# Performance work log

Measured on AMD Instinct MI355X. Metric: run time of the kernel, lower is better.

## Reference

```python
import jax, jax.numpy as jnp
import numpy as np

BN_EPS = 1e-5
NUM_GRAPHS = 64

def _bn(h, gamma, beta):
    # BatchNorm1d over node dim, training-mode (batch statistics, biased var)
    mu = jnp.mean(h, axis=0)
    var = jnp.mean(jnp.square(h - mu), axis=0)
    return gamma * (h - mu) * jax.lax.rsqrt(var + BN_EPS) + beta

def _gin_conv(x, src, dst, Wa, ba, gamma, beta, Wb, bb):
    # sum-aggregate neighbor features: agg[v] = sum_{(u,v) in E} x[u]
    n = x.shape[0]
    agg = jax.ops.segment_sum(x[src], dst, num_segments=n)
    h = x + agg  # eps = 0 (default GINConv)
    h = jax.nn.relu(_bn(h @ Wa + ba, gamma, beta))
    return jax.nn.relu(h @ Wb + bb)

def setup_inputs() -> dict:
    key = jax.random.key(0)
    ks = jax.random.split(key, 16)
    N, E, IN, D, OUT = 50000, 800000, 128, 512, 10
    x = jax.random.normal(ks[0], (N, IN), dtype=jnp.float32)
    edge_index = jax.random.randint(ks[1], (2, E), 0, N, dtype=jnp.int64)
    batch = jnp.sort(jax.random.randint(ks[2], (N,), 0, NUM_GRAPHS, dtype=jnp.int64))
    def lin(k, i, o):
        return jax.random.normal(k, (i, o), dtype=jnp.float32) / np.sqrt(i)
    return {
        "x": x, "edge_index": edge_index, "batch": batch,
        "W1a": lin(ks[3], IN, D), "b1a": jnp.zeros((D,), jnp.float32),
        "g1": jnp.ones((D,), jnp.float32), "be1": jnp.zeros((D,), jnp.float32),
        "W1b": lin(ks[4], D, D), "b1b": jnp.zeros((D,), jnp.float32),
        "W2a": lin(ks[5], D, D), "b2a": jnp.zeros((D,), jnp.float32),
        "g2": jnp.ones((D,), jnp.float32), "be2": jnp.zeros((D,), jnp.float32),
        "W2b": lin(ks[6], D, D), "b2b": jnp.zeros((D,), jnp.float32),
        "Wl1": lin(ks[7], D, D), "bl1": jnp.zeros((D,), jnp.float32),
        "Wl2": lin(ks[8], D, OUT), "bl2": jnp.zeros((OUT,), jnp.float32),
    }

def reference(x, edge_index, batch, W1a, b1a, g1, be1, W1b, b1b,
              W2a, b2a, g2, be2, W2b, b2b, Wl1, bl1, Wl2, bl2):
    src, dst = edge_index[0], edge_index[1]
    h = _gin_conv(x, src, dst, W1a, b1a, g1, be1, W1b, b1b)
    h = _gin_conv(h, src, dst, W2a, b2a, g2, be2, W2b, b2b)
    pooled = jax.ops.segment_sum(h, batch, num_segments=NUM_GRAPHS)  # [G, D]
    out = jax.nn.relu(pooled @ Wl1 + bl1)
    return out @ Wl2 + bl2  # [G, out_channels]
```

## Files before the change

### kernel.cpp

```cpp
#include <hip/hip_runtime.h>
#include <cstdint>
#include <cstddef>

#define N_NODES  50000
#define N_EDGES  800000
#define DIM_IN   128
#define DIM_H    512
#define N_GRAPHS 64
#define DIM_OUT  10
#define BN_EPS   1e-5f
#define SCAN_B   196

typedef _Float16 h16;
using f16x8 = __attribute__((ext_vector_type(8))) _Float16;
using f32x4 = __attribute__((ext_vector_type(4))) float;

__device__ inline float4 add4(float4 a, float4 b) {
    return make_float4(a.x + b.x, a.y + b.y, a.z + b.z, a.w + b.w);
}

__global__ __launch_bounds__(256) void k_wcast_all(
    const float* __restrict__ W1a, const float* __restrict__ W1b,
    const float* __restrict__ W2a, const float* __restrict__ W2b,
    h16* __restrict__ Wt1a, h16* __restrict__ Wt1b,
    h16* __restrict__ Wt2a, h16* __restrict__ Wt2b)
{
    int b = blockIdx.x;
    const float* W; h16* Wt; int K, base;
    if (b < 32)       { W = W1a; Wt = Wt1a; K = DIM_IN; base = 0; }
    else if (b < 160) { W = W1b; Wt = Wt1b; K = DIM_H;  base = 32; }
    else if (b < 288) { W = W2a; Wt = Wt2a; K = DIM_H;  base = 160; }
    else              { W = W2b; Wt = Wt2b; K = DIM_H;  base = 288; }
    int t = (b - base) * 256 + threadIdx.x;
    int total = (K >> 3) * DIM_H;
    if (t >= total) return;
    int k8 = t / DIM_H;
    int n  = t - k8 * DIM_H;
    f16x8 o;
#pragma unroll
    for (int j = 0; j < 8; ++j)
        o[j] = (h16)W[(size_t)(k8 * 8 + j) * DIM_H + n];
    *reinterpret_cast<f16x8*>(&Wt[(size_t)n * K + k8 * 8]) = o;
}

__global__ __launch_bounds__(256) void k_deg(
    const int* __restrict__ dst, int* __restrict__ deg)
{
    int t = blockIdx.x * 256 + threadIdx.x;
    if (t < N_EDGES) atomicAdd(&deg[dst[t]], 1);
}

__global__ __launch_bounds__(256) void k_scan1(
    const int* __restrict__ deg, int* __restrict__ bsum)
{
    __shared__ int s[256];
    int tid = threadIdx.x;
    int i = blockIdx.x * 256 + tid;
    s[tid] = (i < N_NODES) ? deg[i] : 0;
    __syncthreads();
    for (int off = 128; off > 0; off >>= 1) {
        if (tid < off) s[tid] += s[tid + off];
        __syncthreads();
    }
    if (tid == 0) bsum[blockIdx.x] = s[0];
}

__global__ __launch_bounds__(256) void k_scan2(
    const int* __restrict__ bsum, int* __restrict__ boff)
{
    __shared__ int s[256];
    int tid = threadIdx.x;
    s[tid] = (tid < SCAN_B) ? bsum[tid] : 0;
    __syncthreads();
    for (int off = 1; off < 256; off <<= 1) {
        int u = (tid >= off) ? s[tid - off] : 0;
        __syncthreads();
        s[tid] += u;
        __syncthreads();
    }
    if (tid < SCAN_B) boff[tid] = (tid == 0) ? 0 : s[tid - 1];
}

__global__ __launch_bounds__(256) void k_scan3(
    const int* __restrict__ deg, const int* __restrict__ boff,
    int* __restrict__ rowptr, int* __restrict__ cursor)
{
    __shared__ int s[256];
    int tid = threadIdx.x;
    int i = blockIdx.x * 256 + tid;
    int v = (i < N_NODES) ? deg[i] : 0;
    s[tid] = v;
    __syncthreads();
    for (int off = 1; off < 256; off <<= 1) {
        int u = (tid >= off) ? s[tid - off] : 0;
        __syncthreads();
        s[tid] += u;
        __syncthreads();
    }
    int excl = s[tid] - v + boff[blockIdx.x];
    if (i < N_NODES) {
        rowptr[i] = excl;
        cursor[i] = excl;
        if (i == N_NODES - 1) rowptr[N_NODES] = excl + v;
    }
}

__global__ __launch_bounds__(256) void k_fill(
    const int* __restrict__ src, const int* __restrict__ dst,
    int* __restrict__ cursor, int* __restrict__ eidx)
{
    int t = blockIdx.x * 256 + threadIdx.x;
    if (t >= N_EDGES) return;
    int pos = atomicAdd(&cursor[dst[t]], 1);
    eidx[pos] = src[t];
}

__global__ __launch_bounds__(256) void k_gather128(
    const float4* __restrict__ X, const int* __restrict__ rowptr,
    const int* __restrict__ eidx, f16x8* __restrict__ out)
{
    int t = blockIdx.x * 256 + threadIdx.x;
    int v = t >> 4, lane = t & 15;
    if (v >= N_NODES) return;
    int r0 = rowptr[v], r1 = rowptr[v + 1];
    float4 a0 = X[(size_t)v * 32 + lane * 2];
    float4 a1 = X[(size_t)v * 32 + lane * 2 + 1];
    for (int j = r0; j < r1; ++j) {
        int s = eidx[j];
        a0 = add4(a0, X[(size_t)s * 32 + lane * 2]);
        a1 = add4(a1, X[(size_t)s * 32 + lane * 2 + 1]);
    }
    f16x8 o;
    o[0] = (h16)a0.x; o[1] = (h16)a0.y; o[2] = (h16)a0.z; o[3] = (h16)a0.w;
    o[4] = (h16)a1.x; o[5] = (h16)a1.y; o[6] = (h16)a1.z; o[7] = (h16)a1.w;
    out[(size_t)v * 16 + lane] = o;
}

__global__ __launch_bounds__(256) void k_gather512h(
    const f16x8* __restrict__ X, const int* __restrict__ rowptr,
    const int* __restrict__ eidx, f16x8* __restrict__ out)
{
    int t = blockIdx.x * 256 + threadIdx.x;
    int v = t >> 6, lane = t & 63;
    if (v >= N_NODES) return;
    int r0 = rowptr[v], r1 = rowptr[v + 1];
    f16x8 sv = X[(size_t)v * 64 + lane];
    float a[8];
#pragma unroll
    for (int i = 0; i < 8; ++i) a[i] = (float)sv[i];
    int j = r0;
    for (; j + 7 < r1; j += 8) {
        f16x8 b0 = X[(size_t)eidx[j]     * 64 + lane];
        f16x8 b1 = X[(size_t)eidx[j + 1] * 64 + lane];
        f16x8 b2 = X[(size_t)eidx[j + 2] * 64 + lane];
        f16x8 b3 = X[(size_t)eidx[j + 3] * 64 + lane];
        f16x8 b4 = X[(size_t)eidx[j + 4] * 64 + lane];
        f16x8 b5 = X[(size_t)eidx[j + 5] * 64 + lane];
        f16x8 b6 = X[(size_t)eidx[j + 6] * 64 + lane];
        f16x8 b7 = X[(size_t)eidx[j + 7] * 64 + lane];
#pragma unroll
        for (int i = 0; i < 8; ++i)
            a[i] += (((float)b0[i] + (float)b1[i]) + ((float)b2[i] + (float)b3[i]))
                  + (((float)b4[i] + (float)b5[i]) + ((float)b6[i] + (float)b7[i]));
    }
    for (; j + 1 < r1; j += 2) {
        f16x8 b0 = X[(size_t)eidx[j]     * 64 + lane];
        f16x8 b1 = X[(size_t)eidx[j + 1] * 64 + lane];
#pragma unroll
        for (int i = 0; i < 8; ++i) a[i] += (float)b0[i] + (float)b1[i];
    }
    if (j < r1) {
        f16x8 b = X[(size_t)eidx[j] * 64 + lane];
#pragma unroll
        for (int i = 0; i < 8; ++i) a[i] += (float)b[i];
    }
    f16x8 o;
#pragma unroll
    for (int i = 0; i < 8; ++i) o[i] = (h16)a[i];
    out[(size_t)v * 64 + lane] = o;
}

template<bool AFFINE, bool RELU, bool STATS>
__global__ __launch_bounds__(512) void k_gemm_mfma(
    const h16* __restrict__ A, const h16* __restrict__ Bt,
    const float* __restrict__ bias, const float* __restrict__ sA,
    const float* __restrict__ cA, h16* __restrict__ C,
    float* __restrict__ csum, float* __restrict__ csq,
    int M, int N, int K, int lda)
{
    __shared__ f16x8 As[2][128 * 4];
    __shared__ f16x8 Bs[2][256 * 4];

    const int tid  = threadIdx.x;
    const int lane = tid & 63;
    const int w    = tid >> 6;
    const int wr   = w >> 2;
    const int wc   = w & 3;
    const int l15  = lane & 15;
    const int lk   = lane >> 4;
    const int m0   = blockIdx.x * 128;
    const int n0   = blockIdx.y * 256;

    const int a_row = tid >> 2;
    const int kb    = tid & 3;
    const int aswz  = kb ^ (a_row & 3);
    int ar = m0 + a_row; if (ar >= M) ar = M - 1;
    const h16* aptr = A + (size_t)ar * lda + kb * 8;
    const int b_col = tid >> 2;
    const int bswz  = kb ^ (b_col & 3);
    const h16* bptr = Bt + (size_t)(n0 + b_col) * K + kb * 8;
    const size_t bstride = (size_t)128 * K;

    f32x4 acc[4][4];
#pragma unroll
    for (int m = 0; m < 4; ++m)
#pragma unroll
        for (int n = 0; n < 4; ++n)
            acc[m][n] = (f32x4){0.f, 0.f, 0.f, 0.f};

    f16x8 av, bw0, bw1;

    auto load_tile = [&](int k0) {
        av  = *reinterpret_cast<const f16x8*>(aptr + k0);
        if (AFFINE) {
            int kk = k0 + kb * 8;
            float4 s0 = *reinterpret_cast<const float4*>(&sA[kk]);
            float4 s1 = *reinterpret_cast<const float4*>(&sA[kk + 4]);
            float4 c0 = *reinterpret_cast<const float4*>(&cA[kk]);
            float4 c1 = *reinterpret_cast<const float4*>(&cA[kk + 4]);
            float sarr[8] = {s0.x, s0.y, s0.z, s0.w, s1.x, s1.y, s1.z, s1.w};
            float carr[8] = {c0.x, c0.y, c0.z, c0.w, c1.x, c1.y, c1.z, c1.w};
#pragma unroll
            for (int i = 0; i < 8; ++i)
                av[i] = (h16)fmaxf(fmaf((float)av[i], sarr[i], carr[i]), 0.f);
        }
        bw0 = *reinterpret_cast<const f16x8*>(bptr + k0);
        bw1 = *reinterpret_cast<const f16x8*>(bptr + bstride + k0);
    };

    load_tile(0);
    int cur = 0;

    for (int k0 = 0; k0 < K; k0 += 32) {
        As[cur][a_row * 4 + aswz]         = av;
        Bs[cur][b_col * 4 + bswz]         = bw0;
        Bs[cur][(b_col + 128) * 4 + bswz] = bw1;
        if (k0 + 32 < K) load_tile(k0 + 32);
        __syncthreads();

        f16x8 af[4], bf[4];
#pragma unroll
        for (int m = 0; m < 4; ++m) {
            int row = wr * 64 + m * 16 + l15;
            af[m] = As[cur][row * 4 + (lk ^ (row & 3))];
        }
#pragma unroll
        for (int n = 0; n < 4; ++n) {
            int col = wc * 64 + n * 16 + l15;
            bf[n] = Bs[cur][col * 4 + (lk ^ (col & 3))];
        }
#pragma unroll
        for (int m = 0; m < 4; ++m)
#pragma unroll
            for (int n = 0; n < 4; ++n)
                acc[m][n] = __builtin_amdgcn_mfma_f32_16x16x32_f16(
                    af[m], bf[n], acc[m][n], 0, 0, 0);
        cur ^= 1;
    }

#pragma unroll
    for (int n = 0; n < 4; ++n) {
        int col = n0 + wc * 64 + n * 16 + l15;
        float bb = bias[col];
        float sp = 0.f, qp = 0.f;
#pragma unroll
        for (int m = 0; m < 4; ++m) {
            int row0 = m0 + wr * 64 + m * 16 + lk * 4;
#pragma unroll
            for (int r = 0; r < 4; ++r) {
                int row = row0 + r;
                if (row < M) {
                    float v = acc[m][n][r] + bb;
                    if (STATS) { sp += v; qp += v * v; }
                    if (RELU) v = fmaxf(v, 0.f);
                    C[(size_t)row * N + col] = (h16)v;
                }
            }
        }
        if (STATS) {
            sp += __shfl_xor(sp, 16); qp += __shfl_xor(qp, 16);
            sp += __shfl_xor(sp, 32); qp += __shfl_xor(qp, 32);
            if (lk == 0) {
                atomicAdd(&csum[col], sp);
                atomicAdd(&csq[col], qp);
            }
        }
    }
}

__global__ void k_fold(const float* __restrict__ csum, const float* __restrict__ csq,
                       const float* __restrict__ g, const float* __restrict__ be,
                       float* __restrict__ sf, float* __restrict__ cf)
{
    int c = threadIdx.x;
    const float invM = 1.0f / (float)N_NODES;
    float mu  = csum[c] * invM;
    float var = csq[c] * invM - mu * mu;
    float s   = g[c] * rsqrtf(var + BN_EPS);
    sf[c] = s;
    cf[c] = be[c] - mu * s;
}

__global__ __launch_bounds__(256) void k_pool(
    const h16* __restrict__ H, const int* __restrict__ batch,
    float* __restrict__ pooled)
{
    __shared__ int bg[128];
    int base = blockIdx.x * 128;
    if (threadIdx.x < 128) {
        int r = base + threadIdx.x;
        bg[threadIdx.x] = (r < N_NODES) ? batch[r] : -1;
    }
    __syncthreads();
    int c0 = threadIdx.x;
    float a0 = 0.f, a1 = 0.f;
    int cur = bg[0];
    for (int r = 0; r < 128; ++r) {
        int g = bg[r];
        if (g < 0) break;
        if (g != cur) {
            atomicAdd(&pooled[cur * DIM_H + c0],       a0);
            atomicAdd(&pooled[cur * DIM_H + c0 + 256], a1);
            a0 = a1 = 0.f;
            cur = g;
        }
        size_t row = (size_t)(base + r);
        a0 += (float)H[row * DIM_H + c0];
        a1 += (float)H[row * DIM_H + c0 + 256];
    }
    if (cur >= 0) {
        atomicAdd(&pooled[cur * DIM_H + c0],       a0);
        atomicAdd(&pooled[cur * DIM_H + c0 + 256], a1);
    }
}

__global__ __launch_bounds__(512) void k_head1(
    const float* __restrict__ pooled, const float* __restrict__ W,
    const float* __restrict__ b, float* __restrict__ q)
{
    __shared__ float row[DIM_H];
    int g = blockIdx.x, c = threadIdx.x;
    row[c] = pooled[(size_t)g * DIM_H + c];
    __syncthreads();
    float acc = 0.f;
    for (int k = 0; k < DIM_H; ++k)
        acc = fmaf(row[k], W[(size_t)k * DIM_H + c], acc);
    q[(size_t)g * DIM_H + c] = fmaxf(acc + b[c], 0.f);
}

__global__ __launch_bounds__(256) void k_head2(
    const float* __restrict__ q, const float* __restrict__ W,
    const float* __restrict__ b, float* __restrict__ out)
{
    int t = blockIdx.x * 256 + threadIdx.x;
    if (t >= N_GRAPHS * DIM_OUT) return;
    int g = t / DIM_OUT, c = t % DIM_OUT;
    float acc = 0.f;
    for (int k = 0; k < DIM_H; ++k)
        acc = fmaf(q[(size_t)g * DIM_H + k], W[(size_t)k * DIM_OUT + c], acc);
    out[t] = acc + b[c];
}

extern "C" void kernel_launch(void* const* d_in, const int* in_sizes, int n_in,
                              void* d_out, int out_size, void* d_ws, size_t ws_size,
                              hipStream_t stream)
{
    const float* x   = (const float*)d_in[0];
    const int*   ei  = (const int*)d_in[1];
    const int*   src = ei;
    const int*   dst = ei + N_EDGES;
    const int*   batch = (const int*)d_in[2];
    const float* W1a = (const float*)d_in[3];
    const float* b1a = (const float*)d_in[4];
    const float* g1  = (const float*)d_in[5];
    const float* be1 = (const float*)d_in[6];
    const float* W1b = (const float*)d_in[7];
    const float* b1b = (const float*)d_in[8];
    const float* W2a = (const float*)d_in[9];
    const float* b2a = (const float*)d_in[10];
    const float* g2  = (const float*)d_in[11];
    const float* be2 = (const float*)d_in[12];
    const float* W2b = (const float*)d_in[13];
    const float* b2b = (const float*)d_in[14];
    const float* Wl1 = (const float*)d_in[15];
    const float* bl1 = (const float*)d_in[16];
    const float* Wl2 = (const float*)d_in[17];
    const float* bl2 = (const float*)d_in[18];

    char* ws = (char*)d_ws;
    const size_t ROW_H = (size_t)N_NODES * DIM_H * 2;

    if (ws_size < 110000000ull) {
        hipMemsetAsync(d_out, 0, (size_t)out_size * 4, stream);
        return;
    }
    h16* B1h = (h16*)(ws + 0);
    h16* B2h = (h16*)(ws + ROW_H);
    h16* XAh = B2h;
    char* cp  = ws + 2 * ROW_H;
    int* deg    = (int*)(cp + 0);
    int* rowptr = (int*)(cp + 200192);
    int* cursor = (int*)(cp + 400384);
    int* eidx   = (int*)(cp + 600576);
    char* sm    = cp + 3800576;
    float* csum   = (float*)(sm + 0);
    float* csq    = (float*)(sm + 2048);
    float* sf     = (float*)(sm + 4096);
    float* cf     = (float*)(sm + 6144);
    float* pooled = (float*)(sm + 8192);
    float* qbuf   = (float*)(sm + 8192 + 131072);
    char* wt = sm + 8192 + 2 * 131072;
    h16* Wt1a = (h16*)(wt);
    h16* Wt1b = (h16*)(wt + 131072);
    h16* Wt2a = (h16*)(wt + 131072 + 524288);
    h16* Wt2b = (h16*)(wt + 131072 + 2 * 524288);
    int* bsum = (int*)(wt + 131072 + 3 * 524288);
    int* boff = bsum + 256;

    const dim3 gemm_grid(391, 2);
    const int EB = (N_EDGES + 255) / 256;

    k_wcast_all<<<416, 256, 0, stream>>>(W1a, W1b, W2a, W2b,
                                         Wt1a, Wt1b, Wt2a, Wt2b);

    hipMemsetAsync(deg, 0, (size_t)N_NODES * 4, stream);
    k_deg<<<EB, 256, 0, stream>>>(dst, deg);
    k_scan1<<<SCAN_B, 256, 0, stream>>>(deg, bsum);
    k_scan2<<<1, 256, 0, stream>>>(bsum, boff);
    k_scan3<<<SCAN_B, 256, 0, stream>>>(deg, boff, rowptr, cursor);
    k_fill<<<EB, 256, 0, stream>>>(src, dst, cursor, eidx);

    k_gather128<<<(N_NODES * 16 + 255) / 256, 256, 0, stream>>>(
        (const float4*)x, rowptr, eidx, (f16x8*)XAh);
    hipMemsetAsync(csum, 0, 4096, stream);
    k_gemm_mfma<false, false, true><<<gemm_grid, 512, 0, stream>>>(
        XAh, Wt1a, b1a, nullptr, nullptr, B1h, csum, csq,
        N_NODES, DIM_H, DIM_IN, DIM_IN);
    k_fold<<<1, 512, 0, stream>>>(csum, csq, g1, be1, sf, cf);
    k_gemm_mfma<true, true, false><<<gemm_grid, 512, 0, stream>>>(
        B1h, Wt1b, b1b, sf, cf, B2h, nullptr, nullptr,
        N_NODES, DIM_H, DIM_H, DIM_H);

    k_gather512h<<<(N_NODES * 64) / 256, 256, 0, stream>>>(
        (const f16x8*)B2h, rowptr, eidx, (f16x8*)B1h);
    hipMemsetAsync(csum, 0, 4096, stream);
    k_gemm_mfma<false, false, true><<<gemm_grid, 512, 0, stream>>>(
        B1h, Wt2a, b2a, nullptr, nullptr, B2h, csum, csq,
        N_NODES, DIM_H, DIM_H, DIM_H);
    k_fold<<<1, 512, 0, stream>>>(csum, csq, g2, be2, sf, cf);
    k_gemm_mfma<true, true, false><<<gemm_grid, 512, 0, stream>>>(
        B2h, Wt2b, b2b, sf, cf, B1h, nullptr, nullptr,
        N_NODES, DIM_H, DIM_H, DIM_H);

    hipMemsetAsync(pooled, 0, (size_t)N_GRAPHS * DIM_H * 4, stream);
    k_pool<<<(N_NODES + 127) / 128, 256, 0, stream>>>(B1h, batch, pooled);
    k_head1<<<N_GRAPHS, 512, 0, stream>>>(pooled, Wl1, bl1, qbuf);
    k_head2<<<3, 256, 0, stream>>>(qbuf, Wl2, bl2, (float*)d_out);
}
```

Before: 643.5 us.

## Use direct global-to-LDS loads in GEMM and split BN affine into separate kernel

Measured after the change: 653.3 us. No clear change (+1.5%).

```diff
diff --git a/kernel.cpp b/kernel.cpp
--- a/kernel.cpp
+++ b/kernel.cpp
@@ -17,6 +17,12 @@
 
 __device__ inline float4 add4(float4 a, float4 b) {
     return make_float4(a.x + b.x, a.y + b.y, a.z + b.z, a.w + b.w);
+}
+
+__device__ inline void gll16(const void* g, void* l) {
+    __builtin_amdgcn_global_load_lds(
+        (const __attribute__((address_space(1))) void*)g,
+        (__attribute__((address_space(3))) void*)l, 16, 0, 0);
 }
 
 __global__ __launch_bounds__(256) void k_wcast_all(
@@ -180,16 +186,34 @@
     out[(size_t)v * 64 + lane] = o;
 }
 
-template<bool AFFINE, bool RELU, bool STATS>
+__global__ __launch_bounds__(256) void k_affine(
+    h16* __restrict__ T, const float* __restrict__ sf, const float* __restrict__ cf)
+{
+    int t = blockIdx.x * 256 + threadIdx.x;
+    if (t >= N_NODES * (DIM_H / 8)) return;
+    int col0 = (t & 63) * 8;
+    f16x8 v = *reinterpret_cast<const f16x8*>(&T[(size_t)t * 8]);
+    float4 s0 = *reinterpret_cast<const float4*>(&sf[col0]);
+    float4 s1 = *reinterpret_cast<const float4*>(&sf[col0 + 4]);
+    float4 c0 = *reinterpret_cast<const float4*>(&cf[col0]);
+    float4 c1 = *reinterpret_cast<const float4*>(&cf[col0 + 4]);
+    float sarr[8] = {s0.x, s0.y, s0.z, s0.w, s1.x, s1.y, s1.z, s1.w};
+    float carr[8] = {c0.x, c0.y, c0.z, c0.w, c1.x, c1.y, c1.z, c1.w};
+#pragma unroll
+    for (int i = 0; i < 8; ++i)
+        v[i] = (h16)fmaxf(fmaf((float)v[i], sarr[i], carr[i]), 0.f);
+    *reinterpret_cast<f16x8*>(&T[(size_t)t * 8]) = v;
+}
+
+template<bool RELU, bool STATS>
 __global__ __launch_bounds__(512) void k_gemm_mfma(
     const h16* __restrict__ A, const h16* __restrict__ Bt,
-    const float* __restrict__ bias, const float* __restrict__ sA,
-    const float* __restrict__ cA, h16* __restrict__ C,
+    const float* __restrict__ bias, h16* __restrict__ C,
     float* __restrict__ csum, float* __restrict__ csq,
     int M, int N, int K, int lda)
 {
-    __shared__ f16x8 As[2][128 * 4];
-    __shared__ f16x8 Bs[2][256 * 4];
+    __shared__ f16x8 As[128 * 4];
+    __shared__ f16x8 Bs[256 * 4];
 
     const int tid  = threadIdx.x;
     const int lane = tid & 63;
@@ -201,15 +225,22 @@
     const int m0   = blockIdx.x * 128;
     const int n0   = blockIdx.y * 256;
 
-    const int a_row = tid >> 2;
-    const int kb    = tid & 3;
-    const int aswz  = kb ^ (a_row & 3);
+    int sA_ = w * 64 + lane;
+    int a_row = sA_ >> 2;
+    int a_kb  = (sA_ & 3) ^ (a_row & 3);
     int ar = m0 + a_row; if (ar >= M) ar = M - 1;
-    const h16* aptr = A + (size_t)ar * lda + kb * 8;
-    const int b_col = tid >> 2;
-    const int bswz  = kb ^ (b_col & 3);
-    const h16* bptr = Bt + (size_t)(n0 + b_col) * K + kb * 8;
-    const size_t bstride = (size_t)128 * K;
+    const h16* aSrc = A + (size_t)ar * lda + a_kb * 8;
+    f16x8* aBase = &As[w * 64];
+    int sB1 = w * 64 + lane;
+    int b1_col = sB1 >> 2;
+    int b1_kb  = (sB1 & 3) ^ (b1_col & 3);
+    const h16* bSrc1 = Bt + (size_t)(n0 + b1_col) * K + b1_kb * 8;
+    f16x8* bBase1 = &Bs[w * 64];
+    int sB2 = 512 + w * 64 + lane;
+    int b2_col = sB2 >> 2;
+    int b2_kb  = (sB2 & 3) ^ (b2_col & 3);
+    const h16* bSrc2 = Bt + (size_t)(n0 + b2_col) * K + b2_kb * 8;
+    f16x8* bBase2 = &Bs[512 + w * 64];
 
     f32x4 acc[4][4];
 #pragma unroll
@@ -218,46 +249,23 @@
         for (int n = 0; n < 4; ++n)
             acc[m][n] = (f32x4){0.f, 0.f, 0.f, 0.f};
 
-    f16x8 av, bw0, bw1;
-
-    auto load_tile = [&](int k0) {
-        av  = *reinterpret_cast<const f16x8*>(aptr + k0);
-        if (AFFINE) {
-            int kk = k0 + kb * 8;
-            float4 s0 = *reinterpret_cast<const float4*>(&sA[kk]);
-            float4 s1 = *reinterpret_cast<const float4*>(&sA[kk + 4]);
-            float4 c0 = *reinterpret_cast<const float4*>(&cA[kk]);
-            float4 c1 = *reinterpret_cast<const float4*>(&cA[kk + 4]);
-            float sarr[8] = {s0.x, s0.y, s0.z, s0.w, s1.x, s1.y, s1.z, s1.w};
-            float carr[8] = {c0.x, c0.y, c0.z, c0.w, c1.x, c1.y, c1.z, c1.w};
-#pragma unroll
-            for (int i = 0; i < 8; ++i)
-                av[i] = (h16)fmaxf(fmaf((float)av[i], sarr[i], carr[i]), 0.f);
-        }
-        bw0 = *reinterpret_cast<const f16x8*>(bptr + k0);
-        bw1 = *reinterpret_cast<const f16x8*>(bptr + bstride + k0);
-    };
-
-    load_tile(0);
-    int cur = 0;
-
     for (int k0 = 0; k0 < K; k0 += 32) {
-        As[cur][a_row * 4 + aswz]         = av;
-        Bs[cur][b_col * 4 + bswz]         = bw0;
-        Bs[cur][(b_col + 128) * 4 + bswz] = bw1;
-        if (k0 + 32 < K) load_tile(k0 + 32);
+        __syncthreads();
+        gll16(aSrc + k0, aBase);
+        gll16(bSrc1 + k0, bBase1);
+        gll16(bSrc2 + k0, bBase2);
         __syncthreads();
 
         f16x8 af[4], bf[4];
 #pragma unroll
         for (int m = 0; m < 4; ++m) {
             int row = wr * 64 + m * 16 + l15;
-            af[m] = As[cur][row * 4 + (lk ^ (row & 3))];
+            af[m] = As[row * 4 + (lk ^ (row & 3))];
         }
 #pragma unroll
         for (int n = 0; n < 4; ++n) {
             int col = wc * 64 + n * 16 + l15;
-            bf[n] = Bs[cur][col * 4 + (lk ^ (col & 3))];
+            bf[n] = Bs[col * 4 + (lk ^ (col & 3))];
         }
 #pragma unroll
         for (int m = 0; m < 4; ++m)
@@ -265,7 +273,6 @@
             for (int n = 0; n < 4; ++n)
                 acc[m][n] = __builtin_amdgcn_mfma_f32_16x16x32_f16(
                     af[m], bf[n], acc[m][n], 0, 0, 0);
-        cur ^= 1;
     }
 
 #pragma unroll
@@ -429,6 +436,7 @@
 
     const dim3 gemm_grid(391, 2);
     const int EB = (N_EDGES + 255) / 256;
+    const int AFB = (N_NODES * (DIM_H / 8) + 255) / 256;
 
     k_wcast_all<<<416, 256, 0, stream>>>(W1a, W1b, W2a, W2b,
                                          Wt1a, Wt1b, Wt2a, Wt2b);
@@ -443,24 +451,22 @@
     k_gather128<<<(N_NODES * 16 + 255) / 256, 256, 0, stream>>>(
         (const float4*)x, rowptr, eidx, (f16x8*)XAh);
     hipMemsetAsync(csum, 0, 4096, stream);
-    k_gemm_mfma<false, false, true><<<gemm_grid, 512, 0, stream>>>(
-        XAh, Wt1a, b1a, nullptr, nullptr, B1h, csum, csq,
-        N_NODES, DIM_H, DIM_IN, DIM_IN);
+    k_gemm_mfma<false, true><<<gemm_grid, 512, 0, stream>>>(
+        XAh, Wt1a, b1a, B1h, csum, csq, N_NODES, DIM_H, DIM_IN, DIM_IN);
     k_fold<<<1, 512, 0, stream>>>(csum, csq, g1, be1, sf, cf);
-    k_gemm_mfma<true, true, false><<<gemm_grid, 512, 0, stream>>>(
-        B1h, Wt1b, b1b, sf, cf, B2h, nullptr, nullptr,
-        N_NODES, DIM_H, DIM_H, DIM_H);
+    k_affine<<<AFB, 256, 0, stream>>>(B1h, sf, cf);
+    k_gemm_mfma<true, false><<<gemm_grid, 512, 0, stream>>>(
+        B1h, Wt1b, b1b, B2h, nullptr, nullptr, N_NODES, DIM_H, DIM_H, DIM_H);
 
     k_gather512h<<<(N_NODES * 64) / 256, 256, 0, stream>>>(
         (const f16x8*)B2h, rowptr, eidx, (f16x8*)B1h);
     hipMemsetAsync(csum, 0, 4096, stream);
-    k_gemm_mfma<false, false, true><<<gemm_grid, 512, 0, stream>>>(
-        B1h, Wt2a, b2a, nullptr, nullptr, B2h, csum, csq,
-        N_NODES, DIM_H, DIM_H, DIM_H);
+    k_gemm_mfma<false, true><<<gemm_grid, 512, 0, stream>>>(
+        B1h, Wt2a, b2a, B2h, csum, csq, N_NODES, DIM_H, DIM_H, DIM_H);
     k_fold<<<1, 512, 0, stream>>>(csum, csq, g2, be2, sf, cf);
-    k_gemm_mfma<true, true, false><<<gemm_grid, 512, 0, stream>>>(
-        B2h, Wt2b, b2b, sf, cf, B1h, nullptr, nullptr,
-        N_NODES, DIM_H, DIM_H, DIM_H);
+    k_affine<<<AFB, 256, 0, stream>>>(B2h, sf, cf);
+    k_gemm_mfma<true, false><<<gemm_grid, 512, 0, stream>>>(
+        B2h, Wt2b, b2b, B1h, nullptr, nullptr, N_NODES, DIM_H, DIM_H, DIM_H);
 
     hipMemsetAsync(pooled, 0, (size_t)N_GRAPHS * DIM_H * 4, stream);
     k_pool<<<(N_NODES + 127) / 128, 256, 0, stream>>>(B1h, batch, pooled);
```

## Load GEMM B tiles directly into LDS and drop double buffering

Applied to the files above, without the earlier changes.

Measured after the change: 653.5 us. No clear change (+1.5%).

```diff
diff --git a/kernel.cpp b/kernel.cpp
--- a/kernel.cpp
+++ b/kernel.cpp
@@ -17,6 +17,12 @@
 
 __device__ inline float4 add4(float4 a, float4 b) {
     return make_float4(a.x + b.x, a.y + b.y, a.z + b.z, a.w + b.w);
+}
+
+__device__ inline void gll16(const void* g, void* l) {
+    __builtin_amdgcn_global_load_lds(
+        (const __attribute__((address_space(1))) void*)g,
+        (__attribute__((address_space(3))) void*)l, 16, 0, 0);
 }
 
 __global__ __launch_bounds__(256) void k_wcast_all(
@@ -188,8 +194,8 @@
     float* __restrict__ csum, float* __restrict__ csq,
     int M, int N, int K, int lda)
 {
-    __shared__ f16x8 As[2][128 * 4];
-    __shared__ f16x8 Bs[2][256 * 4];
+    __shared__ f16x8 As[128 * 4];
+    __shared__ f16x8 Bs[256 * 4];
 
     const int tid  = threadIdx.x;
     const int lane = tid & 63;
@@ -206,10 +212,17 @@
     const int aswz  = kb ^ (a_row & 3);
     int ar = m0 + a_row; if (ar >= M) ar = M - 1;
     const h16* aptr = A + (size_t)ar * lda + kb * 8;
-    const int b_col = tid >> 2;
-    const int bswz  = kb ^ (b_col & 3);
-    const h16* bptr = Bt + (size_t)(n0 + b_col) * K + kb * 8;
-    const size_t bstride = (size_t)128 * K;
+
+    int sB1 = w * 64 + lane;
+    int b1_col = sB1 >> 2;
+    int b1_kb  = (sB1 & 3) ^ (b1_col & 3);
+    const h16* bSrc1 = Bt + (size_t)(n0 + b1_col) * K + b1_kb * 8;
+    f16x8* bBase1 = &Bs[w * 64];
+    int sB2 = 512 + w * 64 + lane;
+    int b2_col = sB2 >> 2;
+    int b2_kb  = (sB2 & 3) ^ (b2_col & 3);
+    const h16* bSrc2 = Bt + (size_t)(n0 + b2_col) * K + b2_kb * 8;
+    f16x8* bBase2 = &Bs[512 + w * 64];
 
     f32x4 acc[4][4];
 #pragma unroll
@@ -218,10 +231,9 @@
         for (int n = 0; n < 4; ++n)
             acc[m][n] = (f32x4){0.f, 0.f, 0.f, 0.f};
 
-    f16x8 av, bw0, bw1;
-
-    auto load_tile = [&](int k0) {
-        av  = *reinterpret_cast<const f16x8*>(aptr + k0);
+    f16x8 av;
+    auto load_a = [&](int k0) {
+        av = *reinterpret_cast<const f16x8*>(aptr + k0);
         if (AFFINE) {
             int kk = k0 + kb * 8;
             float4 s0 = *reinterpret_cast<const float4*>(&sA[kk]);
@@ -234,30 +246,29 @@
             for (int i = 0; i < 8; ++i)
                 av[i] = (h16)fmaxf(fmaf((float)av[i], sarr[i], carr[i]), 0.f);
         }
-        bw0 = *reinterpret_cast<const f16x8*>(bptr + k0);
-        bw1 = *reinterpret_cast<const f16x8*>(bptr + bstride + k0);
     };
 
-    load_tile(0);
-    int cur = 0;
+    load_a(0);
 
     for (int k0 = 0; k0 < K; k0 += 32) {
-        As[cur][a_row * 4 + aswz]         = av;
-        Bs[cur][b_col * 4 + bswz]         = bw0;
-        Bs[cur][(b_col + 128) * 4 + bswz] = bw1;
-        if (k0 + 32 < K) load_tile(k0 + 32);
-        __syncthreads();
+        __syncthreads();
+        As[a_row * 4 + aswz] = av;
+        gll16(bSrc1 + k0, bBase1);
+        gll16(bSrc2 + k0, bBase2);
+        __syncthreads();
+
+        if (k0 + 32 < K) load_a(k0 + 32);
 
         f16x8 af[4], bf[4];
 #pragma unroll
         for (int m = 0; m < 4; ++m) {
             int row = wr * 64 + m * 16 + l15;
-            af[m] = As[cur][row * 4 + (lk ^ (row & 3))];
+            af[m] = As[row * 4 + (lk ^ (row & 3))];
         }
 #pragma unroll
         for (int n = 0; n < 4; ++n) {
             int col = wc * 64 + n * 16 + l15;
-            bf[n] = Bs[cur][col * 4 + (lk ^ (col & 3))];
+            bf[n] = Bs[col * 4 + (lk ^ (col & 3))];
         }
 #pragma unroll
         for (int m = 0; m < 4; ++m)
@@ -265,7 +276,6 @@
             for (int n = 0; n < 4; ++n)
                 acc[m][n] = __builtin_amdgcn_mfma_f32_16x16x32_f16(
                     af[m], bf[n], acc[m][n], 0, 0, 0);
-        cur ^= 1;
     }
 
 #pragma unroll
```

## Fold memsets, BN fold, and pool/head kernels into neighbouring kernels

Applied to the files above, without the earlier changes.

Result: slower. 766.1 us (+19.1%).

```diff
diff --git a/kernel.cpp b/kernel.cpp
--- a/kernel.cpp
+++ b/kernel.cpp
@@ -23,8 +23,12 @@
     const float* __restrict__ W1a, const float* __restrict__ W1b,
     const float* __restrict__ W2a, const float* __restrict__ W2b,
     h16* __restrict__ Wt1a, h16* __restrict__ Wt1b,
-    h16* __restrict__ Wt2a, h16* __restrict__ Wt2b)
-{
+    h16* __restrict__ Wt2a, h16* __restrict__ Wt2b,
+    int* __restrict__ deg)
+{
+    for (int i = blockIdx.x * 256 + threadIdx.x; i < N_NODES; i += 416 * 256)
+        deg[i] = 0;
+
     int b = blockIdx.x;
     const float* W; h16* Wt; int K, base;
     if (b < 32)       { W = W1a; Wt = Wt1a; K = DIM_IN; base = 0; }
@@ -83,7 +87,8 @@
 
 __global__ __launch_bounds__(256) void k_scan3(
     const int* __restrict__ deg, const int* __restrict__ boff,
-    int* __restrict__ rowptr, int* __restrict__ cursor)
+    int* __restrict__ rowptr, int* __restrict__ cursor,
+    float* __restrict__ csum)
 {
     __shared__ int s[256];
     int tid = threadIdx.x;
@@ -103,6 +108,8 @@
         cursor[i] = excl;
         if (i == N_NODES - 1) rowptr[N_NODES] = excl + v;
     }
+    if (blockIdx.x == 0)
+        for (int z = tid; z < 2 * DIM_H; z += 256) csum[z] = 0.f;
 }
 
 __global__ __launch_bounds__(256) void k_fill(
@@ -138,8 +145,12 @@
 
 __global__ __launch_bounds__(256) void k_gather512h(
     const f16x8* __restrict__ X, const int* __restrict__ rowptr,
-    const int* __restrict__ eidx, f16x8* __restrict__ out)
-{
+    const int* __restrict__ eidx, f16x8* __restrict__ out,
+    float* __restrict__ csum)
+{
+    if (blockIdx.x == 0)
+        for (int z = threadIdx.x; z < 2 * DIM_H; z += 256) csum[z] = 0.f;
+
     int t = blockIdx.x * 256 + threadIdx.x;
     int v = t >> 6, lane = t & 63;
     if (v >= N_NODES) return;
@@ -183,13 +194,14 @@
 template<bool AFFINE, bool RELU, bool STATS>
 __global__ __launch_bounds__(512) void k_gemm_mfma(
     const h16* __restrict__ A, const h16* __restrict__ Bt,
-    const float* __restrict__ bias, const float* __restrict__ sA,
-    const float* __restrict__ cA, h16* __restrict__ C,
+    const float* __restrict__ bias,
     float* __restrict__ csum, float* __restrict__ csq,
-    int M, int N, int K, int lda)
-{
-    __shared__ f16x8 As[2][128 * 4];
-    __shared__ f16x8 Bs[2][256 * 4];
+    const float* __restrict__ gam, const float* __restrict__ bet,
+    h16* __restrict__ C, int M, int N, int K, int lda)
+{
+    __shared__ f16x8 As[128 * 4];
+    __shared__ f16x8 Bs[256 * 4];
+    __shared__ float sfl[DIM_H], cfl[DIM_H];
 
     const int tid  = threadIdx.x;
     const int lane = tid & 63;
@@ -201,6 +213,18 @@
     const int m0   = blockIdx.x * 128;
     const int n0   = blockIdx.y * 256;
 
+    if (AFFINE) {
+        const float invM = 1.0f / (float)N_NODES;
+        for (int cc = tid; cc < K; cc += 512) {
+            float mu  = csum[cc] * invM;
+            float var = csq[cc] * invM - mu * mu;
+            float s   = gam[cc] * rsqrtf(var + BN_EPS);
+            sfl[cc] = s;
+            cfl[cc] = bet[cc] - mu * s;
+        }
+        __syncthreads();
+    }
+
     const int a_row = tid >> 2;
     const int kb    = tid & 3;
     const int aswz  = kb ^ (a_row & 3);
@@ -224,10 +248,10 @@
         av  = *reinterpret_cast<const f16x8*>(aptr + k0);
         if (AFFINE) {
             int kk = k0 + kb * 8;
-            float4 s0 = *reinterpret_cast<const float4*>(&sA[kk]);
-            float4 s1 = *reinterpret_cast<const float4*>(&sA[kk + 4]);
-            float4 c0 = *reinterpret_cast<const float4*>(&cA[kk]);
-            float4 c1 = *reinterpret_cast<const float4*>(&cA[kk + 4]);
+            float4 s0 = *reinterpret_cast<const float4*>(&sfl[kk]);
+            float4 s1 = *reinterpret_cast<const float4*>(&sfl[kk + 4]);
+            float4 c0 = *reinterpret_cast<const float4*>(&cfl[kk]);
+            float4 c1 = *reinterpret_cast<const float4*>(&cfl[kk + 4]);
             float sarr[8] = {s0.x, s0.y, s0.z, s0.w, s1.x, s1.y, s1.z, s1.w};
             float carr[8] = {c0.x, c0.y, c0.z, c0.w, c1.x, c1.y, c1.z, c1.w};
 #pragma unroll
@@ -239,25 +263,26 @@
     };
 
     load_tile(0);
-    int cur = 0;
 
     for (int k0 = 0; k0 < K; k0 += 32) {
-        As[cur][a_row * 4 + aswz]         = av;
-        Bs[cur][b_col * 4 + bswz]         = bw0;
-        Bs[cur][(b_col + 128) * 4 + bswz] = bw1;
+        __syncthreads();
+        As[a_row * 4 + aswz]          = av;
+        Bs[b_col * 4 + bswz]          = bw0;
+        Bs[(b_col + 128) * 4 + bswz]  = bw1;
+        __syncthreads();
+
         if (k0 + 32 < K) load_tile(k0 + 32);
-        __syncthreads();
 
         f16x8 af[4], bf[4];
 #pragma unroll
         for (int m = 0; m < 4; ++m) {
             int row = wr * 64 + m * 16 + l15;
-            af[m] = As[cur][row * 4 + (lk ^ (row & 3))];
+            af[m] = As[row * 4 + (lk ^ (row & 3))];
         }
 #pragma unroll
         for (int n = 0; n < 4; ++n) {
             int col = wc * 64 + n * 16 + l15;
-            bf[n] = Bs[cur][col * 4 + (lk ^ (col & 3))];
+            bf[n] = Bs[col * 4 + (lk ^ (col & 3))];
         }
 #pragma unroll
         for (int m = 0; m < 4; ++m)
@@ -265,7 +290,6 @@
             for (int n = 0; n < 4; ++n)
                 acc[m][n] = __builtin_amdgcn_mfma_f32_16x16x32_f16(
                     af[m], bf[n], acc[m][n], 0, 0, 0);
-        cur ^= 1;
     }
 
 #pragma unroll
@@ -298,77 +322,43 @@
     }
 }
 
-__global__ void k_fold(const float* __restrict__ csum, const float* __restrict__ csq,
-                       const float* __restrict__ g, const float* __restrict__ be,
-                       float* __restrict__ sf, float* __restrict__ cf)
-{
-    int c = threadIdx.x;
-    const float invM = 1.0f / (float)N_NODES;
-    float mu  = csum[c] * invM;
-    float var = csq[c] * invM - mu * mu;
-    float s   = g[c] * rsqrtf(var + BN_EPS);
-    sf[c] = s;
-    cf[c] = be[c] - mu * s;
-}
-
-__global__ __launch_bounds__(256) void k_pool(
+__global__ __launch_bounds__(512) void k_poolhead(
     const h16* __restrict__ H, const int* __restrict__ batch,
-    float* __restrict__ pooled)
-{
-    __shared__ int bg[128];
-    int base = blockIdx.x * 128;
-    if (threadIdx.x < 128) {
-        int r = base + threadIdx.x;
-        bg[threadIdx.x] = (r < N_NODES) ? batch[r] : -1;
-    }
-    __syncthreads();
-    int c0 = threadIdx.x;
-    float a0 = 0.f, a1 = 0.f;
-    int cur = bg[0];
-    for (int r = 0; r < 128; ++r) {
-        int g = bg[r];
-        if (g < 0) break;
-        if (g != cur) {
-            atomicAdd(&pooled[cur * DIM_H + c0],       a0);
-            atomicAdd(&pooled[cur * DIM_H + c0 + 256], a1);
-            a0 = a1 = 0.f;
-            cur = g;
-        }
-        size_t row = (size_t)(base + r);
-        a0 += (float)H[row * DIM_H + c0];
-        a1 += (float)H[row * DIM_H + c0 + 256];
-    }
-    if (cur >= 0) {
-        atomicAdd(&pooled[cur * DIM_H + c0],       a0);
-        atomicAdd(&pooled[cur * DIM_H + c0 + 256], a1);
-    }
-}
-
-__global__ __launch_bounds__(512) void k_head1(
-    const float* __restrict__ pooled, const float* __restrict__ W,
-    const float* __restrict__ b, float* __restrict__ q)
-{
-    __shared__ float row[DIM_H];
+    const float* __restrict__ Wl1, const float* __restrict__ bl1,
+    const float* __restrict__ Wl2, const float* __restrict__ bl2,
+    float* __restrict__ out)
+{
+    __shared__ float rowp[DIM_H];
+    __shared__ float qv[DIM_H];
+    __shared__ int bounds[2];
     int g = blockIdx.x, c = threadIdx.x;
-    row[c] = pooled[(size_t)g * DIM_H + c];
+    if (c < 2) {
+        int target = g + c;
+        int lo = 0, hi = N_NODES;
+        while (lo < hi) {
+            int mid = (lo + hi) >> 1;
+            if (batch[mid] < target) lo = mid + 1; else hi = mid;
+        }
+        bounds[c] = lo;
+    }
+    __syncthreads();
+    int r0 = bounds[0], r1 = bounds[1];
+    float s = 0.f;
+    for (int r = r0; r < r1; ++r)
+        s += (float)H[(size_t)r * DIM_H + c];
+    rowp[c] = s;
     __syncthreads();
     float acc = 0.f;
     for (int k = 0; k < DIM_H; ++k)
-        acc = fmaf(row[k], W[(size_t)k * DIM_H + c], acc);
-    q[(size_t)g * DIM_H + c] = fmaxf(acc + b[c], 0.f);
-}
-
-__global__ __launch_bounds__(256) void k_head2(
-    const float* __restrict__ q, const float* __restrict__ W,
-    const float* __restrict__ b, float* __restrict__ out)
-{
-    int t = blockIdx.x * 256 + threadIdx.x;
-    if (t >= N_GRAPHS * DIM_OUT) return;
-    int g = t / DIM_OUT, c = t % DIM_OUT;
-    float acc = 0.f;
-    for (int k = 0; k < DIM_H; ++k)
-        acc = fmaf(q[(size_t)g * DIM_H + k], W[(size_t)k * DIM_OUT + c], acc);
-    out[t] = acc + b[c];
+        acc = fmaf(rowp[k], Wl1[(size_t)k * DIM_H + c], acc);
+    qv[c] = fmaxf(acc + bl1[c], 0.f);
+    __syncthreads();
+    if (c < DIM_OUT) {
+        float a2 = 0.f;
+        for (int k = 0; k < DIM_H; ++k)
+            a2 = fmaf(qv[k], Wl2[(size_t)k * DIM_OUT + c], a2);
+        out[g * DIM_OUT + c] = a2 + bl2[c];
+    }
 }
 
 extern "C" void kernel_launch(void* const* d_in, const int* in_sizes, int n_in,
@@ -415,11 +405,7 @@
     char* sm    = cp + 3800576;
     float* csum   = (float*)(sm + 0);
     float* csq    = (float*)(sm + 2048);
-    float* sf     = (float*)(sm + 4096);
-    float* cf     = (float*)(sm + 6144);
-    float* pooled = (float*)(sm + 8192);
-    float* qbuf   = (float*)(sm + 8192 + 131072);
-    char* wt = sm + 8192 + 2 * 131072;
+    char* wt = sm + 8192;
     h16* Wt1a = (h16*)(wt);
     h16* Wt1b = (h16*)(wt + 131072);
     h16* Wt2a = (h16*)(wt + 131072 + 524288);
@@ -431,39 +417,31 @@
     const int EB = (N_EDGES + 255) / 256;
 
     k_wcast_all<<<416, 256, 0, stream>>>(W1a, W1b, W2a, W2b,
-                                         Wt1a, Wt1b, Wt2a, Wt2b);
-
-    hipMemsetAsync(deg, 0, (size_t)N_NODES * 4, stream);
+                                         Wt1a, Wt1b, Wt2a, Wt2b, deg);
     k_deg<<<EB, 256, 0, stream>>>(dst, deg);
     k_scan1<<<SCAN_B, 256, 0, stream>>>(deg, bsum);
     k_scan2<<<1, 256, 0, stream>>>(bsum, boff);
-    k_scan3<<<SCAN_B, 256, 0, stream>>>(deg, boff, rowptr, cursor);
+    k_scan3<<<SCAN_B, 256, 0, stream>>>(deg, boff, rowptr, cursor, csum);
     k_fill<<<EB, 256, 0, stream>>>(src, dst, cursor, eidx);
 
     k_gather128<<<(N_NODES * 16 + 255) / 256, 256, 0, stream>>>(
         (const float4*)x, rowptr, eidx, (f16x8*)XAh);
-    hipMemsetAsync(csum, 0, 4096, stream);
     k_gemm_mfma<false, false, true><<<gemm_grid, 512, 0, stream>>>(
-        XAh, Wt1a, b1a, nullptr, nullptr, B1h, csum, csq,
+        XAh, Wt1a, b1a, csum, csq, nullptr, nullptr, B1h,
         N_NODES, DIM_H, DIM_IN, DIM_IN);
-    k_fold<<<1, 512, 0, stream>>>(csum, csq, g1, be1, sf, cf);
     k_gemm_mfma<true, true, false><<<gemm_grid, 512, 0, stream>>>(
-        B1h, Wt1b, b1b, sf, cf, B2h, nullptr, nullptr,
+        B1h, Wt1b, b1b, csum, csq, g1, be1, B2h,
         N_NODES, DIM_H, DIM_H, DIM_H);
 
     k_gather512h<<<(N_NODES * 64) / 256, 256, 0, stream>>>(
-        (const f16x8*)B2h, rowptr, eidx, (f16x8*)B1h);
-    hipMemsetAsync(csum, 0, 4096, stream);
+        (const f16x8*)B2h, rowptr, eidx, (f16x8*)B1h, csum);
     k_gemm_mfma<false, false, true><<<gemm_grid, 512, 0, stream>>>(
-        B1h, Wt2a, b2a, nullptr, nullptr, B2h, csum, csq,
+        B1h, Wt2a, b2a, csum, csq, nullptr, nullptr, B2h,
         N_NODES, DIM_H, DIM_H, DIM_H);
-    k_fold<<<1, 512, 0, stream>>>(csum, csq, g2, be2, sf, cf);
     k_gemm_mfma<true, true, false><<<gemm_grid, 512, 0, stream>>>(
-        B2h, Wt2b, b2b, sf, cf, B1h, nullptr, nullptr,
+        B2h, Wt2b, b2b, csum, csq, g2, be2, B1h,
         N_NODES, DIM_H, DIM_H, DIM_H);
 
-    hipMemsetAsync(pooled, 0, (size_t)N_GRAPHS * DIM_H * 4, stream);
-    k_pool<<<(N_NODES + 127) / 128, 256, 0, stream>>>(B1h, batch, pooled);
-    k_head1<<<N_GRAPHS, 512, 0, stream>>>(pooled, Wl1, bl1, qbuf);
-    k_head2<<<3, 256, 0, stream>>>(qbuf, Wl2, bl2, (float*)d_out);
-}
+    k_poolhead<<<N_GRAPHS, 512, 0, stream>>>(
+        B1h, batch, Wl1, bl1, Wl2, bl2, (float*)d_out);
+}
```
